# Kernel tuning notes

Measured on AMD Instinct MI355X. Metric: run time of the kernel, lower is better.

Reference implementation:

```python
import jax, jax.numpy as jnp
import numpy as np


def setup_inputs() -> dict:
    key = jax.random.key(0)
    ks = jax.random.split(key, 4)
    B, L, D, H, C = 32, 512, 768, 100, 45
    sequence_output = jax.random.normal(ks[0], (B, L, D), dtype=jnp.float32)
    valid_ids = jax.random.randint(ks[1], (B, L), 0, 2, dtype=jnp.int32)
    W1 = jax.random.normal(ks[2], (H, D), dtype=jnp.float32) * 0.02
    b1 = jnp.zeros((H,), jnp.float32)
    W2 = jax.random.normal(ks[3], (C, H), dtype=jnp.float32) * 0.02
    b2 = jnp.zeros((C,), jnp.float32)
    return {"sequence_output": sequence_output, "valid_ids": valid_ids,
            "W1": W1, "b1": b1, "W2": W2, "b2": b2}


def reference(sequence_output, valid_ids, W1, b1, W2, b2):
    # Vectorized equivalent of the nested compaction loop:
    # for each row i, valid tokens (valid_ids==1) are packed to the front,
    # remaining slots stay zero.
    B, L, D = sequence_output.shape
    valid = valid_ids == 1                      # [B, L] bool
    pos = jnp.cumsum(valid, axis=1) - 1         # destination index for valid tokens
    pos = jnp.where(valid, pos, L)              # invalid tokens -> dump slot L
    bidx = jnp.arange(B)[:, None]               # [B, 1]
    buf = jnp.zeros((B, L + 1, D), sequence_output.dtype)
    buf = buf.at[bidx, pos].set(sequence_output)  # scatter rows in parallel
    valid_output = buf[:, :L]                   # drop the dump slot
    # Dropout (p=0.3, training) in the original is stochastic; omitted here
    # (identity / eval mode) so the baseline is deterministic.
    h = valid_output @ W1.T + b1                # [B, L, 100]
    logits = h @ W2.T + b2                      # [B, L, num_labels]
    return logits.reshape(-1, W2.shape[0])      # [B*L, num_labels]
```

## Files before the change

kernel.cpp:

```cpp
#include <hip/hip_runtime.h>
#include <hip/hip_bf16.h>
#include <stdint.h>

#define Bb 32
#define Ll 512
#define Dd 768
#define Hh 100
#define Cc 45
#define CP 48
#define MROWS (Bb * Ll)

typedef __attribute__((ext_vector_type(8))) short short8;
typedef __attribute__((ext_vector_type(4))) float f32x4;

__device__ __forceinline__ unsigned short f2bf_rne(float v) {
    uint32_t u = __float_as_uint(v);
    return (unsigned short)((u + 0x7fffu + ((u >> 16) & 1u)) >> 16);
}

__global__ void prep_wc(const float* __restrict__ W1, const float* __restrict__ b1,
                        const float* __restrict__ W2, const float* __restrict__ b2,
                        unsigned short* __restrict__ Wc, float* __restrict__ bc) {
    int c = blockIdx.x;
    int t = threadIdx.x;
    if (c >= Cc) {
        for (int i = t; i < Dd; i += 256) Wc[c * Dd + i] = 0;
        if (t == 0) bc[c] = 0.f;
        return;
    }
    float a0 = 0.f, a1 = 0.f, a2 = 0.f;
    const int d0 = t, d1 = t + 256, d2 = t + 512;
    for (int h = 0; h < Hh; ++h) {
        float w2 = W2[c * Hh + h];
        a0 += w2 * W1[h * Dd + d0];
        a1 += w2 * W1[h * Dd + d1];
        a2 += w2 * W1[h * Dd + d2];
    }
    Wc[c * Dd + d0] = f2bf_rne(a0);
    Wc[c * Dd + d1] = f2bf_rne(a1);
    Wc[c * Dd + d2] = f2bf_rne(a2);
    if (t == 0) {
        float s = b2[c];
        for (int h = 0; h < Hh; ++h) s += W2[c * Hh + h] * b1[h];
        bc[c] = s;
    }
}

__global__ void prep_gather(const int* __restrict__ valid, int* __restrict__ gather) {
    int b = blockIdx.x;
    int t = threadIdx.x;
    __shared__ int s[Ll];
    int v = (valid[b * Ll + t] == 1) ? 1 : 0;
    s[t] = v;
    gather[b * Ll + t] = -1;
    __syncthreads();
    for (int off = 1; off < Ll; off <<= 1) {
        int x = (t >= off) ? s[t - off] : 0;
        __syncthreads();
        s[t] += x;
        __syncthreads();
    }
    if (v) gather[b * Ll + (s[t] - 1)] = b * Ll + t;
}

__global__ __launch_bounds__(256) void gemm_out(
    const float* __restrict__ x,
    const unsigned short* __restrict__ Wc,
    const float* __restrict__ bc,
    const int* __restrict__ gather,
    float* __restrict__ out)
{
    const int wave = threadIdx.x >> 6;
    const int lane = threadIdx.x & 63;
    const int quad = lane >> 4;
    const int nn   = lane & 15;
    const int rowbase = (blockIdx.x * 4 + wave) * 16;

    const int src = gather[rowbase + nn];
    const float* xp = x + (long)(src >= 0 ? src : 0) * Dd + quad * 8;

    const unsigned short* bp0 = Wc + (0 * 16 + nn) * Dd + quad * 8;
    const unsigned short* bp1 = Wc + (1 * 16 + nn) * Dd + quad * 8;
    const unsigned short* bp2 = Wc + (2 * 16 + nn) * Dd + quad * 8;

    f32x4 acc0 = {0.f, 0.f, 0.f, 0.f};
    f32x4 acc1 = {0.f, 0.f, 0.f, 0.f};
    f32x4 acc2 = {0.f, 0.f, 0.f, 0.f};

    #pragma unroll 6
    for (int ks = 0; ks < 24; ++ks) {
        union { short8 s; uint32_t u[4]; } A;
        A.u[0] = 0; A.u[1] = 0; A.u[2] = 0; A.u[3] = 0;
        if (src >= 0) {
            f32x4 xa = *(const f32x4*)(xp + ks * 32);
            f32x4 xb = *(const f32x4*)(xp + ks * 32 + 4);
            A.u[0] = (__float_as_uint(xa.x) >> 16) | (__float_as_uint(xa.y) & 0xffff0000u);
            A.u[1] = (__float_as_uint(xa.z) >> 16) | (__float_as_uint(xa.w) & 0xffff0000u);
            A.u[2] = (__float_as_uint(xb.x) >> 16) | (__float_as_uint(xb.y) & 0xffff0000u);
            A.u[3] = (__float_as_uint(xb.z) >> 16) | (__float_as_uint(xb.w) & 0xffff0000u);
        }
        short8 b0 = *(const short8*)(bp0 + ks * 32);
        short8 b1v = *(const short8*)(bp1 + ks * 32);
        short8 b2v = *(const short8*)(bp2 + ks * 32);
        acc0 = __builtin_amdgcn_mfma_f32_16x16x32_bf16(A.s, b0,  acc0, 0, 0, 0);
        acc1 = __builtin_amdgcn_mfma_f32_16x16x32_bf16(A.s, b1v, acc1, 0, 0, 0);
        acc2 = __builtin_amdgcn_mfma_f32_16x16x32_bf16(A.s, b2v, acc2, 0, 0, 0);
    }

    #pragma unroll
    for (int ct = 0; ct < 3; ++ct) {
        int col = ct * 16 + nn;
        if (col < Cc) {
            float bcv = bc[col];
            f32x4 acc = (ct == 0) ? acc0 : ((ct == 1) ? acc1 : acc2);
            #pragma unroll
            for (int r = 0; r < 4; ++r) {
                int row = rowbase + quad * 4 + r;
                out[row * Cc + col] = acc[r] + bcv;
            }
        }
    }
}

extern "C" void kernel_launch(void* const* d_in, const int* in_sizes, int n_in,
                              void* d_out, int out_size, void* d_ws, size_t ws_size,
                              hipStream_t stream) {
    const float* seq   = (const float*)d_in[0];
    const int*   valid = (const int*)d_in[1];
    const float* W1    = (const float*)d_in[2];
    const float* b1    = (const float*)d_in[3];
    const float* W2    = (const float*)d_in[4];
    const float* b2    = (const float*)d_in[5];
    float* out = (float*)d_out;

    unsigned short* Wc = (unsigned short*)d_ws;
    float* bc          = (float*)((char*)d_ws + 73728);
    int* gather        = (int*)((char*)d_ws + 73728 + 192);

    prep_wc<<<CP, 256, 0, stream>>>(W1, b1, W2, b2, Wc, bc);
    prep_gather<<<Bb, Ll, 0, stream>>>(valid, gather);
    gemm_out<<<MROWS / 64, 256, 0, stream>>>(seq, Wc, bc, gather, out);
}
```

Measured before the change: 121.4 us.

## Fuse compaction scan into GEMM and split K across waves with LDS reduction

```diff
diff --git a/kernel.cpp b/kernel.cpp
--- a/kernel.cpp
+++ b/kernel.cpp
@@ -21,74 +21,81 @@
 __global__ void prep_wc(const float* __restrict__ W1, const float* __restrict__ b1,
                         const float* __restrict__ W2, const float* __restrict__ b2,
                         unsigned short* __restrict__ Wc, float* __restrict__ bc) {
-    int c = blockIdx.x;
-    int t = threadIdx.x;
+    const int c     = blockIdx.x / 3;
+    const int chunk = blockIdx.x % 3;
+    const int t     = threadIdx.x;
+    const int d     = chunk * 256 + t;
     if (c >= Cc) {
-        for (int i = t; i < Dd; i += 256) Wc[c * Dd + i] = 0;
-        if (t == 0) bc[c] = 0.f;
-        return;
+        Wc[c * Dd + d] = 0;
+    } else {
+        float a = 0.f;
+        const float* w1p = W1 + d;
+        const float* w2p = W2 + c * Hh;
+        #pragma unroll 4
+        for (int h = 0; h < Hh; ++h) a += w2p[h] * w1p[h * Dd];
+        Wc[c * Dd + d] = f2bf_rne(a);
     }
-    float a0 = 0.f, a1 = 0.f, a2 = 0.f;
-    const int d0 = t, d1 = t + 256, d2 = t + 512;
-    for (int h = 0; h < Hh; ++h) {
-        float w2 = W2[c * Hh + h];
-        a0 += w2 * W1[h * Dd + d0];
-        a1 += w2 * W1[h * Dd + d1];
-        a2 += w2 * W1[h * Dd + d2];
-    }
-    Wc[c * Dd + d0] = f2bf_rne(a0);
-    Wc[c * Dd + d1] = f2bf_rne(a1);
-    Wc[c * Dd + d2] = f2bf_rne(a2);
-    if (t == 0) {
-        float s = b2[c];
-        for (int h = 0; h < Hh; ++h) s += W2[c * Hh + h] * b1[h];
-        bc[c] = s;
+    if (blockIdx.x == 0 && t < CP) {
+        float s = (t < Cc) ? b2[t] : 0.f;
+        if (t < Cc)
+            for (int h = 0; h < Hh; ++h) s += W2[t * Hh + h] * b1[h];
+        bc[t] = s;
     }
 }
 
-__global__ void prep_gather(const int* __restrict__ valid, int* __restrict__ gather) {
-    int b = blockIdx.x;
-    int t = threadIdx.x;
-    __shared__ int s[Ll];
-    int v = (valid[b * Ll + t] == 1) ? 1 : 0;
-    s[t] = v;
-    gather[b * Ll + t] = -1;
-    __syncthreads();
-    for (int off = 1; off < Ll; off <<= 1) {
-        int x = (t >= off) ? s[t - off] : 0;
-        __syncthreads();
-        s[t] += x;
-        __syncthreads();
-    }
-    if (v) gather[b * Ll + (s[t] - 1)] = b * Ll + t;
-}
-
-__global__ __launch_bounds__(256) void gemm_out(
+__global__ __launch_bounds__(256, 4) void gemm_out(
     const float* __restrict__ x,
+    const int* __restrict__ valid,
     const unsigned short* __restrict__ Wc,
     const float* __restrict__ bc,
-    const int* __restrict__ gather,
     float* __restrict__ out)
 {
-    const int wave = threadIdx.x >> 6;
-    const int lane = threadIdx.x & 63;
+    __shared__ int   g[Ll];
+    __shared__ int   wsum[4];
+    __shared__ float red[4][12][64];
+
+    const int t    = threadIdx.x;
+    const int wave = t >> 6;
+    const int lane = t & 63;
     const int quad = lane >> 4;
     const int nn   = lane & 15;
-    const int rowbase = (blockIdx.x * 4 + wave) * 16;
 
-    const int src = gather[rowbase + nn];
-    const float* xp = x + (long)(src >= 0 ? src : 0) * Dd + quad * 8;
+    const int rowbase = blockIdx.x * 16;
+    const int b       = rowbase >> 9;
+    const int p0      = rowbase & (Ll - 1);
 
-    const unsigned short* bp0 = Wc + (0 * 16 + nn) * Dd + quad * 8;
-    const unsigned short* bp1 = Wc + (1 * 16 + nn) * Dd + quad * 8;
-    const unsigned short* bp2 = Wc + (2 * 16 + nn) * Dd + quad * 8;
+    g[t] = -1; g[t + 256] = -1;
+    int2 vv = ((const int2*)(valid + b * Ll))[t];
+    int v0 = (vv.x == 1), v1 = (vv.y == 1);
+    int ps = v0 + v1;
+    __syncthreads();
+    int incl = ps;
+    #pragma unroll
+    for (int d = 1; d < 64; d <<= 1) {
+        int n = __shfl_up(incl, d, 64);
+        if (lane >= d) incl += n;
+    }
+    if (lane == 63) wsum[wave] = incl;
+    __syncthreads();
+    int woff = 0;
+    #pragma unroll
+    for (int w = 0; w < 4; ++w) woff += (w < wave) ? wsum[w] : 0;
+    int e = woff + incl - ps;
+    if (v0) g[e] = 2 * t;
+    if (v1) g[e + v0] = 2 * t + 1;
+    __syncthreads();
+
+    const int srcl = g[p0 + nn];
+    const int src  = (srcl >= 0) ? (b * Ll + srcl) : -1;
+    const float* xp = x + (long)(src >= 0 ? src : 0) * Dd + wave * 192 + quad * 8;
+    const unsigned short* bp = Wc + nn * Dd + wave * 192 + quad * 8;
 
     f32x4 acc0 = {0.f, 0.f, 0.f, 0.f};
     f32x4 acc1 = {0.f, 0.f, 0.f, 0.f};
     f32x4 acc2 = {0.f, 0.f, 0.f, 0.f};
 
-    #pragma unroll 6
-    for (int ks = 0; ks < 24; ++ks) {
+    #pragma unroll
+    for (int ks = 0; ks < 6; ++ks) {
         union { short8 s; uint32_t u[4]; } A;
         A.u[0] = 0; A.u[1] = 0; A.u[2] = 0; A.u[3] = 0;
         if (src >= 0) {
@@ -99,25 +106,33 @@
             A.u[2] = (__float_as_uint(xb.x) >> 16) | (__float_as_uint(xb.y) & 0xffff0000u);
             A.u[3] = (__float_as_uint(xb.z) >> 16) | (__float_as_uint(xb.w) & 0xffff0000u);
         }
-        short8 b0 = *(const short8*)(bp0 + ks * 32);
-        short8 b1v = *(const short8*)(bp1 + ks * 32);
-        short8 b2v = *(const short8*)(bp2 + ks * 32);
+        short8 b0 = *(const short8*)(bp + 0 * 16 * Dd + ks * 32);
+        short8 b1v = *(const short8*)(bp + 1 * 16 * Dd + ks * 32);
+        short8 b2v = *(const short8*)(bp + 2 * 16 * Dd + ks * 32);
         acc0 = __builtin_amdgcn_mfma_f32_16x16x32_bf16(A.s, b0,  acc0, 0, 0, 0);
         acc1 = __builtin_amdgcn_mfma_f32_16x16x32_bf16(A.s, b1v, acc1, 0, 0, 0);
         acc2 = __builtin_amdgcn_mfma_f32_16x16x32_bf16(A.s, b2v, acc2, 0, 0, 0);
     }
 
     #pragma unroll
-    for (int ct = 0; ct < 3; ++ct) {
-        int col = ct * 16 + nn;
+    for (int r = 0; r < 4; ++r) {
+        red[wave][0 * 4 + r][lane] = acc0[r];
+        red[wave][1 * 4 + r][lane] = acc1[r];
+        red[wave][2 * 4 + r][lane] = acc2[r];
+    }
+    __syncthreads();
+
+    #pragma unroll
+    for (int oo = 0; oo < 3; ++oo) {
+        int o = t + oo * 256;
+        int j = o >> 6, l = o & 63;
+        float s = red[0][j][l] + red[1][j][l] + red[2][j][l] + red[3][j][l];
+        int q = l >> 4, n2 = l & 15;
+        int ct = j >> 2, r = j & 3;
+        int col = ct * 16 + n2;
         if (col < Cc) {
-            float bcv = bc[col];
-            f32x4 acc = (ct == 0) ? acc0 : ((ct == 1) ? acc1 : acc2);
-            #pragma unroll
-            for (int r = 0; r < 4; ++r) {
-                int row = rowbase + quad * 4 + r;
-                out[row * Cc + col] = acc[r] + bcv;
-            }
+            int row = rowbase + q * 4 + r;
+            out[row * Cc + col] = s + bc[col];
         }
     }
 }
@@ -135,9 +150,7 @@
 
     unsigned short* Wc = (unsigned short*)d_ws;
     float* bc          = (float*)((char*)d_ws + 73728);
-    int* gather        = (int*)((char*)d_ws + 73728 + 192);
 
-    prep_wc<<<CP, 256, 0, stream>>>(W1, b1, W2, b2, Wc, bc);
-    prep_gather<<<Bb, Ll, 0, stream>>>(valid, gather);
-    gemm_out<<<MROWS / 64, 256, 0, stream>>>(seq, Wc, bc, gather, out);
+    prep_wc<<<CP * 3, 256, 0, stream>>>(W1, b1, W2, b2, Wc, bc);
+    gemm_out<<<MROWS / 16, 256, 0, stream>>>(seq, valid, Wc, bc, out);
 }
```

After: 113.7 us. -6.3%, faster.
